# Optimization experiments

Measured on AMD Instinct MI355X. Metric: run time of the kernel, lower is better.

Reference implementation:

```python
import jax, jax.numpy as jnp
import numpy as np
import math

B, M, V, C, HID, BIN, H, W = 2, 1024, 300, 128, 128, 256, 384, 512


def fibonacci_sphere(n):
    # generate_grasp_views: n approximately-uniform directions on the unit sphere
    i = np.arange(n, dtype=np.float64)
    phi = (np.sqrt(5.0) - 1.0) / 2.0
    z = (2.0 * i + 1.0) / n - 1.0
    r = np.sqrt(np.maximum(1.0 - z * z, 0.0))
    t = 2.0 * np.pi * i * phi
    v = np.stack([r * np.cos(t), r * np.sin(t), z], -1)
    return (v / np.linalg.norm(v, axis=-1, keepdims=True)).astype(np.float32)


def setup_inputs():
    key = jax.random.key(0)
    ks = jax.random.split(key, 24)
    seed_features = jax.random.normal(ks[0], (B, C, M), jnp.float32)
    token_sel_idx = jax.random.randint(ks[1], (B, M), 0, H * W)
    fx = 525.0
    Kmat = jnp.array([[fx, 0.0, W / 2.0], [0.0, fx, H / 2.0], [0.0, 0.0, 1.0]], jnp.float32)
    K = jnp.broadcast_to(Kmat, (B, 3, 3))
    depth_map = 0.2 + 0.8 * jax.random.uniform(ks[2], (B, 1, H, W), jnp.float32)
    depth_prob = jax.nn.softmax(jax.random.normal(ks[3], (B, BIN, H, W), jnp.float32), axis=1)
    view_dirs = jnp.asarray(fibonacci_sphere(V))

    def lin(k, fan_in, shape):
        s = 1.0 / np.sqrt(fan_in)
        return jax.random.uniform(k, shape, jnp.float32, -s, s)

    qin = C + 7  # seed_feat + ray(3) + normal(3) + uncert(1)
    params = dict(
        Wq1=lin(ks[4], qin, (qin, HID)), bq1=lin(ks[5], qin, (HID,)),
        Wq2=lin(ks[6], HID, (HID, HID)), bq2=lin(ks[7], HID, (HID,)),
        Wa1=lin(ks[8], 3, (3, HID)), ba1=lin(ks[9], 3, (HID,)),
        Wa2=lin(ks[10], HID, (HID, HID)), ba2=lin(ks[11], HID, (HID,)),
        Wb1=lin(ks[12], 3, (3, HID // 2)), bb1=lin(ks[13], 3, (HID // 2,)),
        Wb2=lin(ks[14], HID // 2, (HID // 2, 1)), bb2=lin(ks[15], HID // 2, (1,)),
        Wr1=lin(ks[16], HID, (HID, C)), br1=lin(ks[17], HID, (C,)),
        Wr2=lin(ks[18], C, (C, C)), br2=lin(ks[19], C, (C,)),
    )
    return dict(seed_features=seed_features, token_sel_idx=token_sel_idx, K=K,
                depth_map=depth_map, depth_prob=depth_prob, view_dirs=view_dirs, **params)


def _views_to_rot(views):
    # batch_viewpoint_params_to_matrix(-views, angle=0)
    axis_x = -views
    zero = jnp.zeros_like(axis_x[..., 0])
    axis_y = jnp.stack([-axis_x[..., 1], axis_x[..., 0], zero], -1)
    ny = jnp.linalg.norm(axis_y, axis=-1, keepdims=True)
    fallback = jnp.broadcast_to(jnp.array([0.0, 1.0, 0.0], views.dtype), axis_y.shape)
    axis_y = jnp.where(ny < 1e-8, fallback, axis_y / jnp.maximum(ny, 1e-8))
    axis_x = axis_x / jnp.maximum(jnp.linalg.norm(axis_x, axis=-1, keepdims=True), 1e-8)
    axis_z = jnp.cross(axis_x, axis_y)
    return jnp.stack([axis_x, axis_y, axis_z], -1)  # (B,M,3,3)


def _forward(seed_features, token_sel_idx, K, depth_map, depth_prob, view_dirs,
             Wq1, bq1, Wq2, bq2, Wa1, ba1, Wa2, ba2, Wb1, bb1, Wb2, bb2, Wr1, br1, Wr2, br2):
    depth_map = jax.lax.stop_gradient(depth_map)   # .detach() in torch
    depth_prob = jax.lax.stop_gradient(depth_prob)
    # --- backproject depth to xyz map (B,3,H,W) ---
    ys, xs = jnp.meshgrid(jnp.arange(H, dtype=jnp.float32), jnp.arange(W, dtype=jnp.float32), indexing='ij')
    fx = K[:, 0, 0][:, None, None, None]; fy = K[:, 1, 1][:, None, None, None]
    cx = K[:, 0, 2][:, None, None, None]; cy = K[:, 1, 2][:, None, None, None]
    z = depth_map
    x = (xs[None, None] - cx) / fx * z
    y = (ys[None, None] - cy) / fy * z
    xyz = jnp.concatenate([x, y, z], axis=1)
    # --- central-difference normal map with replicate pad ---
    dx = (xyz[:, :, :, 2:] - xyz[:, :, :, :-2])[:, :, 1:-1, :]
    dy = (xyz[:, :, 2:, :] - xyz[:, :, :-2, :])[:, :, :, 1:-1]
    n = jnp.cross(dx.transpose(0, 2, 3, 1), dy.transpose(0, 2, 3, 1))
    n = n / jnp.maximum(jnp.linalg.norm(n, axis=-1, keepdims=True), 1e-6)
    normal_map = jnp.pad(n.transpose(0, 3, 1, 2), ((0, 0), (0, 0), (1, 1), (1, 1)), mode='edge')
    # --- depth uncertainty: normalized entropy over bins ---
    p = jnp.maximum(depth_prob, 1e-8)
    uncert_map = jnp.clip(-(p * jnp.log(p)).sum(axis=1, keepdims=True) / math.log(BIN), 0.0, 1.0)
    # --- per-seed irregular gathers ---
    def gather(feat, idx):
        Bf, Cf = feat.shape[0], feat.shape[1]
        flat = feat.reshape(Bf, Cf, H * W)
        return jnp.take_along_axis(flat, jnp.broadcast_to(idx[:, None, :], (Bf, Cf, idx.shape[1])), axis=2)
    normal_bm3 = gather(normal_map, token_sel_idx).transpose(0, 2, 1)  # (B,M,3)
    uncert_bm1 = gather(uncert_map, token_sel_idx).transpose(0, 2, 1)  # (B,M,1)
    u = (token_sel_idx % W).astype(jnp.float32)
    v = (token_sel_idx // W).astype(jnp.float32)
    rx = (u - K[:, 0, 2][:, None]) / K[:, 0, 0][:, None]
    ry = (v - K[:, 1, 2][:, None]) / K[:, 1, 1][:, None]
    rays = jnp.stack([rx, ry, jnp.ones_like(rx)], -1)
    rays = rays / jnp.maximum(jnp.linalg.norm(rays, axis=-1, keepdims=True), 1e-12)
    normal_bm3 = normal_bm3 * (1.0 - uncert_bm1)
    # --- query / anchor / bias MLPs ---
    q_in = jnp.concatenate([seed_features.transpose(0, 2, 1), rays, normal_bm3, uncert_bm1], -1)
    q = jax.nn.relu(jax.nn.relu(q_in @ Wq1 + bq1) @ Wq2 + bq2)          # (B,M,HID)
    a = jax.nn.relu(view_dirs @ Wa1 + ba1) @ Wa2 + ba2                  # (V,HID)
    bias = (jax.nn.relu(view_dirs @ Wb1 + bb1) @ Wb2 + bb2)[:, 0]        # (V,)
    logits = jnp.einsum('bmh,vh->bmv', q, a) / jnp.sqrt(jnp.float32(HID)) + bias
    view_score = jax.nn.sigmoid(logits)                                  # (B,M,V)
    # --- top-1 view selection + gather xyz / rot / anchor feat ---
    top_inds = jnp.argmax(view_score, axis=-1)                           # (B,M)
    top_xyz = view_dirs[top_inds]                                        # (B,M,3)
    rot = _views_to_rot(top_xyz)                                         # (B,M,3,3)
    top_a = a[top_inds]                                                  # (B,M,HID)
    res = jax.nn.relu((q + top_a) @ Wr1 + br1) @ Wr2 + br2               # (B,M,C)
    res_feat = res.transpose(0, 2, 1)                                    # (B,C,M)
    return view_score, top_inds, top_xyz, rot, res_feat


def reference(seed_features, token_sel_idx, K, depth_map, depth_prob, view_dirs,
              Wq1, bq1, Wq2, bq2, Wa1, ba1, Wa2, ba2, Wb1, bb1, Wb2, bb2, Wr1, br1, Wr2, br2):
    return _forward(seed_features, token_sel_idx, K, depth_map, depth_prob, view_dirs,
                    Wq1, bq1, Wq2, bq2, Wa1, ba1, Wa2, ba2, Wb1, bb1, Wb2, bb2, Wr1, br1, Wr2, br2)
```

## Files before the change

### kernel.cpp

```cpp
#include <hip/hip_runtime.h>
#include <math.h>

#define B 2
#define M 1024
#define V 300
#define C 128
#define HID 128
#define BIN 256
#define H 384
#define W 512
#define QIN (C + 7)
#define TM 8

__global__ __launch_bounds__(HID) void anchor_kernel(
    const float* __restrict__ view_dirs,
    const float* __restrict__ Wa1, const float* __restrict__ ba1,
    const float* __restrict__ Wa2, const float* __restrict__ ba2,
    const float* __restrict__ Wb1, const float* __restrict__ bb1,
    const float* __restrict__ Wb2, const float* __restrict__ bb2,
    float* __restrict__ a_out, float* __restrict__ aT_out,
    float* __restrict__ bias_out) {
  const int v = blockIdx.x;
  const int t = threadIdx.x;
  __shared__ float h1[HID];

  const float vd0 = view_dirs[v * 3 + 0];
  const float vd1 = view_dirs[v * 3 + 1];
  const float vd2 = view_dirs[v * 3 + 2];

  float h = vd0 * Wa1[0 * HID + t] + vd1 * Wa1[1 * HID + t] + vd2 * Wa1[2 * HID + t] + ba1[t];
  h1[t] = fmaxf(h, 0.0f);

  if (t < 64) {
    float x = vd0 * Wb1[0 * 64 + t] + vd1 * Wb1[1 * 64 + t] + vd2 * Wb1[2 * 64 + t] + bb1[t];
    x = fmaxf(x, 0.0f) * Wb2[t];
#pragma unroll
    for (int o = 32; o > 0; o >>= 1) x += __shfl_down(x, o, 64);
    if (t == 0) bias_out[v] = x + bb2[0];
  }
  __syncthreads();

  float acc = ba2[t];
#pragma unroll 8
  for (int k = 0; k < HID; ++k) acc += h1[k] * Wa2[k * HID + t];
  a_out[v * HID + t] = acc;
  aT_out[(size_t)t * V + v] = acc;
}

__global__ __launch_bounds__(256) void seed_kernel(
    const float* __restrict__ seed_features, const int* __restrict__ token_sel_idx,
    const float* __restrict__ Kmat, const float* __restrict__ depth_map,
    const float* __restrict__ depth_prob, const float* __restrict__ view_dirs,
    const float* __restrict__ Wq1, const float* __restrict__ bq1,
    const float* __restrict__ Wq2, const float* __restrict__ bq2,
    const float* __restrict__ Wr1, const float* __restrict__ br1,
    const float* __restrict__ Wr2, const float* __restrict__ br2,
    const float* __restrict__ a_ws, const float* __restrict__ aT_ws,
    const float* __restrict__ bias_ws,
    float* __restrict__ out_view_score, float* __restrict__ out_top_inds,
    float* __restrict__ out_top_xyz, float* __restrict__ out_rot,
    float* __restrict__ out_res) {
  const int bm0 = blockIdx.x * TM;
  const int b = bm0 / M;
  const int m0 = bm0 - b * M;
  const int t = threadIdx.x;
  const int lane = t & 63;
  const int wv = t >> 6;

  __shared__ float qin[TM][QIN + 1];
  __shared__ float hs[TM][HID];
  __shared__ float qs[TM][HID];
  __shared__ float sc_s[TM][304];
  __shared__ float atop[TM][HID];
  __shared__ float ered[TM];
  __shared__ int   sidx[TM];
  __shared__ int   sbest[TM];

  if (t < TM) sidx[t] = token_sel_idx[bm0 + t];

  for (int i = t; i < TM * C; i += 256) {
    const int s = i & 7;
    const int c = i >> 3;
    qin[s][c] = seed_features[((size_t)b * C + c) * M + m0 + s];
  }
  __syncthreads();

  {
    const int es = t >> 5;
    const int sub = t & 31;
    const float* dp = depth_prob + (size_t)b * BIN * H * W + sidx[es];
    float e = 0.0f;
#pragma unroll
    for (int j = 0; j < 8; ++j) {
      const float p = fmaxf(dp[(size_t)(sub + 32 * j) * (H * W)], 1e-8f);
      e += p * logf(p);
    }
#pragma unroll
    for (int o = 16; o > 0; o >>= 1) e += __shfl_down(e, o, 32);
    if (sub == 0) ered[es] = e;
  }
  __syncthreads();

  if (t < TM) {
    const int idx = sidx[t];
    float uncert = (-ered[t]) / 5.5451774444795623f;
    uncert = fminf(fmaxf(uncert, 0.0f), 1.0f);

    const float fx = Kmat[b * 9 + 0], fy = Kmat[b * 9 + 4];
    const float cx = Kmat[b * 9 + 2], cy = Kmat[b * 9 + 5];
    const int w = idx % W;
    const int h = idx / W;
    const int hc = min(max(h, 1), H - 2);
    const int wc = min(max(w, 1), W - 2);

    const float* dm = depth_map + (size_t)b * H * W;
    const float zl = dm[hc * W + (wc - 1)];
    const float zr = dm[hc * W + (wc + 1)];
    const float zu = dm[(hc - 1) * W + wc];
    const float zd = dm[(hc + 1) * W + wc];

    const float dxx = (wc + 1 - cx) / fx * zr - (wc - 1 - cx) / fx * zl;
    const float dxy = (hc - cy) / fy * zr - (hc - cy) / fy * zl;
    const float dxz = zr - zl;
    const float dyx = (wc - cx) / fx * zd - (wc - cx) / fx * zu;
    const float dyy = (hc + 1 - cy) / fy * zd - (hc - 1 - cy) / fy * zu;
    const float dyz = zd - zu;

    float nx = dxy * dyz - dxz * dyy;
    float ny = dxz * dyx - dxx * dyz;
    float nz = dxx * dyy - dxy * dyx;
    const float nn = fmaxf(sqrtf(nx * nx + ny * ny + nz * nz), 1e-6f);
    const float sc = (1.0f - uncert) / nn;

    const float rx = ((float)w - cx) / fx;
    const float ry = ((float)h - cy) / fy;
    const float rn = fmaxf(sqrtf(rx * rx + ry * ry + 1.0f), 1e-12f);

    qin[t][128] = rx / rn;
    qin[t][129] = ry / rn;
    qin[t][130] = 1.0f / rn;
    qin[t][131] = nx * sc;
    qin[t][132] = ny * sc;
    qin[t][133] = nz * sc;
    qin[t][134] = uncert;
  }
  __syncthreads();

  const int col = t & 127;
  const int grp = (t >> 7) * 4;
  {
    float acc0 = bq1[col], acc1 = acc0, acc2 = acc0, acc3 = acc0;
#pragma unroll 5
    for (int i = 0; i < QIN; ++i) {
      const float w = Wq1[i * HID + col];
      acc0 += qin[grp + 0][i] * w;
      acc1 += qin[grp + 1][i] * w;
      acc2 += qin[grp + 2][i] * w;
      acc3 += qin[grp + 3][i] * w;
    }
    hs[grp + 0][col] = fmaxf(acc0, 0.0f);
    hs[grp + 1][col] = fmaxf(acc1, 0.0f);
    hs[grp + 2][col] = fmaxf(acc2, 0.0f);
    hs[grp + 3][col] = fmaxf(acc3, 0.0f);
  }
  __syncthreads();

  {
    float acc0 = bq2[col], acc1 = acc0, acc2 = acc0, acc3 = acc0;
#pragma unroll 8
    for (int k = 0; k < HID; ++k) {
      const float w = Wq2[k * HID + col];
      acc0 += hs[grp + 0][k] * w;
      acc1 += hs[grp + 1][k] * w;
      acc2 += hs[grp + 2][k] * w;
      acc3 += hs[grp + 3][k] * w;
    }
    qs[grp + 0][col] = fmaxf(acc0, 0.0f);
    qs[grp + 1][col] = fmaxf(acc1, 0.0f);
    qs[grp + 2][col] = fmaxf(acc2, 0.0f);
    qs[grp + 3][col] = fmaxf(acc3, 0.0f);
  }
  __syncthreads();

  const float rsq = 0.08838834764831845f;
  for (int v = t; v < V; v += 256) {
    float d[TM];
#pragma unroll
    for (int s = 0; s < TM; ++s) d[s] = 0.0f;
#pragma unroll 4
    for (int k = 0; k < HID; ++k) {
      const float av = aT_ws[(size_t)k * V + v];
#pragma unroll
      for (int s = 0; s < TM; ++s) d[s] += qs[s][k] * av;
    }
    const float bsv = bias_ws[v];
#pragma unroll
    for (int s = 0; s < TM; ++s) {
      const float scv = 1.0f / (1.0f + expf(-(d[s] * rsq + bsv)));
      sc_s[s][v] = scv;
      out_view_score[(size_t)(bm0 + s) * V + v] = scv;
    }
  }
  __syncthreads();

  for (int s = wv; s < TM; s += 4) {
    float bv = -1.0f;
    int bi = 0;
    for (int v = lane; v < V; v += 64) {
      const float x = sc_s[s][v];
      if (x > bv) { bv = x; bi = v; }
    }
#pragma unroll
    for (int o = 32; o > 0; o >>= 1) {
      const float ov = __shfl_down(bv, o, 64);
      const int oi = __shfl_down(bi, o, 64);
      if (ov > bv || (ov == bv && oi < bi)) { bv = ov; bi = oi; }
    }
    if (lane == 0) sbest[s] = bi;
  }
  __syncthreads();

  if (t < TM) {
    const int best = sbest[t];
    const int bm = bm0 + t;
    out_top_inds[bm] = (float)best;
    const float vx = view_dirs[best * 3 + 0];
    const float vy = view_dirs[best * 3 + 1];
    const float vz = view_dirs[best * 3 + 2];
    out_top_xyz[(size_t)bm * 3 + 0] = vx;
    out_top_xyz[(size_t)bm * 3 + 1] = vy;
    out_top_xyz[(size_t)bm * 3 + 2] = vz;

    float ax0 = -vx, ax1 = -vy, ax2 = -vz;
    float ay0 = vy, ay1 = -vx, ay2 = 0.0f;
    const float nyn = sqrtf(ay0 * ay0 + ay1 * ay1);
    if (nyn < 1e-8f) {
      ay0 = 0.0f; ay1 = 1.0f; ay2 = 0.0f;
    } else {
      const float d = fmaxf(nyn, 1e-8f);
      ay0 /= d; ay1 /= d;
    }
    const float an = fmaxf(sqrtf(ax0 * ax0 + ax1 * ax1 + ax2 * ax2), 1e-8f);
    ax0 /= an; ax1 /= an; ax2 /= an;
    const float az0 = ax1 * ay2 - ax2 * ay1;
    const float az1 = ax2 * ay0 - ax0 * ay2;
    const float az2 = ax0 * ay1 - ax1 * ay0;
    float* R = out_rot + (size_t)bm * 9;
    R[0] = ax0; R[1] = ay0; R[2] = az0;
    R[3] = ax1; R[4] = ay1; R[5] = az1;
    R[6] = ax2; R[7] = ay2; R[8] = az2;
  }

  for (int i = t; i < TM * HID; i += 256) {
    const int s = i >> 7;
    const int k = i & 127;
    atop[s][k] = a_ws[(size_t)sbest[s] * HID + k];
  }
  __syncthreads();

  {
    float acc0 = br1[col], acc1 = acc0, acc2 = acc0, acc3 = acc0;
#pragma unroll 8
    for (int k = 0; k < HID; ++k) {
      const float w = Wr1[k * HID + col];
      acc0 += (qs[grp + 0][k] + atop[grp + 0][k]) * w;
      acc1 += (qs[grp + 1][k] + atop[grp + 1][k]) * w;
      acc2 += (qs[grp + 2][k] + atop[grp + 2][k]) * w;
      acc3 += (qs[grp + 3][k] + atop[grp + 3][k]) * w;
    }
    hs[grp + 0][col] = fmaxf(acc0, 0.0f);
    hs[grp + 1][col] = fmaxf(acc1, 0.0f);
    hs[grp + 2][col] = fmaxf(acc2, 0.0f);
    hs[grp + 3][col] = fmaxf(acc3, 0.0f);
  }
  __syncthreads();

  {
    float acc0 = br2[col], acc1 = acc0, acc2 = acc0, acc3 = acc0;
#pragma unroll 8
    for (int k = 0; k < HID; ++k) {
      const float w = Wr2[k * HID + col];
      acc0 += hs[grp + 0][k] * w;
      acc1 += hs[grp + 1][k] * w;
      acc2 += hs[grp + 2][k] * w;
      acc3 += hs[grp + 3][k] * w;
    }
    float* o = out_res + ((size_t)b * C + col) * M + m0 + grp;
    o[0] = acc0; o[1] = acc1; o[2] = acc2; o[3] = acc3;
  }
}

extern "C" void kernel_launch(void* const* d_in, const int* in_sizes, int n_in,
                              void* d_out, int out_size, void* d_ws, size_t ws_size,
                              hipStream_t stream) {
  const float* seed  = (const float*)d_in[0];
  const int*   tok   = (const int*)d_in[1];
  const float* Km    = (const float*)d_in[2];
  const float* dmap  = (const float*)d_in[3];
  const float* dprob = (const float*)d_in[4];
  const float* vdirs = (const float*)d_in[5];
  const float* Wq1 = (const float*)d_in[6];  const float* bq1 = (const float*)d_in[7];
  const float* Wq2 = (const float*)d_in[8];  const float* bq2 = (const float*)d_in[9];
  const float* Wa1 = (const float*)d_in[10]; const float* ba1 = (const float*)d_in[11];
  const float* Wa2 = (const float*)d_in[12]; const float* ba2 = (const float*)d_in[13];
  const float* Wb1 = (const float*)d_in[14]; const float* bb1 = (const float*)d_in[15];
  const float* Wb2 = (const float*)d_in[16]; const float* bb2 = (const float*)d_in[17];
  const float* Wr1 = (const float*)d_in[18]; const float* br1 = (const float*)d_in[19];
  const float* Wr2 = (const float*)d_in[20]; const float* br2 = (const float*)d_in[21];

  float* out = (float*)d_out;
  float* vs  = out;
  float* ti  = vs + (size_t)B * M * V;
  float* tx  = ti + (size_t)B * M;
  float* rot = tx + (size_t)B * M * 3;
  float* rf  = rot + (size_t)B * M * 9;

  float* a_ws    = (float*)d_ws;
  float* aT_ws   = a_ws + (size_t)V * HID;
  float* bias_ws = aT_ws + (size_t)HID * V;

  anchor_kernel<<<V, HID, 0, stream>>>(vdirs, Wa1, ba1, Wa2, ba2, Wb1, bb1, Wb2, bb2,
                                       a_ws, aT_ws, bias_ws);
  seed_kernel<<<(B * M) / TM, 256, 0, stream>>>(seed, tok, Km, dmap, dprob, vdirs,
                                                Wq1, bq1, Wq2, bq2, Wr1, br1, Wr2, br2,
                                                a_ws, aT_ws, bias_ws, vs, ti, tx, rot, rf);
}
```

Baseline: 558.4 us.

## Split depth-entropy and geometry computation into a separate per-seed kernel

Moves the depth-probability entropy, surface normal and ray computation out of the MLP kernel into a new geo_kernel with one 256-thread block per seed. Each thread does one strided gather of depth_prob, which gives far more blocks and memory parallelism for these scattered loads than the 8-seeds-per-block layout did. The MLP kernel now reads the 7 extra features from a workspace buffer. This adds a kernel launch and a small round trip through global memory.

```diff
diff --git a/kernel.cpp b/kernel.cpp
--- a/kernel.cpp
+++ b/kernel.cpp
@@ -11,6 +11,76 @@
 #define W 512
 #define QIN (C + 7)
 #define TM 8
+
+__global__ __launch_bounds__(256) void geo_kernel(
+    const int* __restrict__ token_sel_idx, const float* __restrict__ Kmat,
+    const float* __restrict__ depth_map, const float* __restrict__ depth_prob,
+    float* __restrict__ extras) {
+  const int bm = blockIdx.x;
+  const int b = bm >> 10;
+  const int t = threadIdx.x;
+  const int lane = t & 63;
+  const int wv = t >> 6;
+
+  __shared__ float ered[4];
+  __shared__ int sidx_s;
+  if (t == 0) sidx_s = token_sel_idx[bm];
+  __syncthreads();
+  const int idx = sidx_s;
+
+  {
+    const float p = fmaxf(depth_prob[(size_t)b * BIN * H * W + (size_t)t * (H * W) + idx], 1e-8f);
+    float e = p * logf(p);
+#pragma unroll
+    for (int o = 32; o > 0; o >>= 1) e += __shfl_down(e, o, 64);
+    if (lane == 0) ered[wv] = e;
+  }
+  __syncthreads();
+
+  if (t == 0) {
+    float uncert = (-(ered[0] + ered[1] + ered[2] + ered[3])) / 5.5451774444795623f;
+    uncert = fminf(fmaxf(uncert, 0.0f), 1.0f);
+
+    const float fx = Kmat[b * 9 + 0], fy = Kmat[b * 9 + 4];
+    const float cx = Kmat[b * 9 + 2], cy = Kmat[b * 9 + 5];
+    const int w = idx % W;
+    const int h = idx / W;
+    const int hc = min(max(h, 1), H - 2);
+    const int wc = min(max(w, 1), W - 2);
+
+    const float* dm = depth_map + (size_t)b * H * W;
+    const float zl = dm[hc * W + (wc - 1)];
+    const float zr = dm[hc * W + (wc + 1)];
+    const float zu = dm[(hc - 1) * W + wc];
+    const float zd = dm[(hc + 1) * W + wc];
+
+    const float dxx = (wc + 1 - cx) / fx * zr - (wc - 1 - cx) / fx * zl;
+    const float dxy = (hc - cy) / fy * zr - (hc - cy) / fy * zl;
+    const float dxz = zr - zl;
+    const float dyx = (wc - cx) / fx * zd - (wc - cx) / fx * zu;
+    const float dyy = (hc + 1 - cy) / fy * zd - (hc - 1 - cy) / fy * zu;
+    const float dyz = zd - zu;
+
+    float nx = dxy * dyz - dxz * dyy;
+    float ny = dxz * dyx - dxx * dyz;
+    float nz = dxx * dyy - dxy * dyx;
+    const float nn = fmaxf(sqrtf(nx * nx + ny * ny + nz * nz), 1e-6f);
+    const float sc = (1.0f - uncert) / nn;
+
+    const float rx = ((float)w - cx) / fx;
+    const float ry = ((float)h - cy) / fy;
+    const float rn = fmaxf(sqrtf(rx * rx + ry * ry + 1.0f), 1e-12f);
+
+    float* e8 = extras + (size_t)bm * 8;
+    e8[0] = rx / rn;
+    e8[1] = ry / rn;
+    e8[2] = 1.0f / rn;
+    e8[3] = nx * sc;
+    e8[4] = ny * sc;
+    e8[5] = nz * sc;
+    e8[6] = uncert;
+  }
+}
 
 __global__ __launch_bounds__(HID) void anchor_kernel(
     const float* __restrict__ view_dirs,
@@ -47,10 +117,9 @@
   aT_out[(size_t)t * V + v] = acc;
 }
 
-__global__ __launch_bounds__(256) void seed_kernel(
-    const float* __restrict__ seed_features, const int* __restrict__ token_sel_idx,
-    const float* __restrict__ Kmat, const float* __restrict__ depth_map,
-    const float* __restrict__ depth_prob, const float* __restrict__ view_dirs,
+__global__ __launch_bounds__(256) void seed_mlp_kernel(
+    const float* __restrict__ seed_features, const float* __restrict__ extras,
+    const float* __restrict__ view_dirs,
     const float* __restrict__ Wq1, const float* __restrict__ bq1,
     const float* __restrict__ Wq2, const float* __restrict__ bq2,
     const float* __restrict__ Wr1, const float* __restrict__ br1,
@@ -61,7 +130,7 @@
     float* __restrict__ out_top_xyz, float* __restrict__ out_rot,
     float* __restrict__ out_res) {
   const int bm0 = blockIdx.x * TM;
-  const int b = bm0 / M;
+  const int b = bm0 >> 10;
   const int m0 = bm0 - b * M;
   const int t = threadIdx.x;
   const int lane = t & 63;
@@ -72,82 +141,23 @@
   __shared__ float qs[TM][HID];
   __shared__ float sc_s[TM][304];
   __shared__ float atop[TM][HID];
-  __shared__ float ered[TM];
-  __shared__ int   sidx[TM];
   __shared__ int   sbest[TM];
-
-  if (t < TM) sidx[t] = token_sel_idx[bm0 + t];
 
   for (int i = t; i < TM * C; i += 256) {
     const int s = i & 7;
     const int c = i >> 3;
     qin[s][c] = seed_features[((size_t)b * C + c) * M + m0 + s];
   }
-  __syncthreads();
-
-  {
-    const int es = t >> 5;
-    const int sub = t & 31;
-    const float* dp = depth_prob + (size_t)b * BIN * H * W + sidx[es];
-    float e = 0.0f;
-#pragma unroll
-    for (int j = 0; j < 8; ++j) {
-      const float p = fmaxf(dp[(size_t)(sub + 32 * j) * (H * W)], 1e-8f);
-      e += p * logf(p);
-    }
-#pragma unroll
-    for (int o = 16; o > 0; o >>= 1) e += __shfl_down(e, o, 32);
-    if (sub == 0) ered[es] = e;
-  }
-  __syncthreads();
-
-  if (t < TM) {
-    const int idx = sidx[t];
-    float uncert = (-ered[t]) / 5.5451774444795623f;
-    uncert = fminf(fmaxf(uncert, 0.0f), 1.0f);
-
-    const float fx = Kmat[b * 9 + 0], fy = Kmat[b * 9 + 4];
-    const float cx = Kmat[b * 9 + 2], cy = Kmat[b * 9 + 5];
-    const int w = idx % W;
-    const int h = idx / W;
-    const int hc = min(max(h, 1), H - 2);
-    const int wc = min(max(w, 1), W - 2);
-
-    const float* dm = depth_map + (size_t)b * H * W;
-    const float zl = dm[hc * W + (wc - 1)];
-    const float zr = dm[hc * W + (wc + 1)];
-    const float zu = dm[(hc - 1) * W + wc];
-    const float zd = dm[(hc + 1) * W + wc];
-
-    const float dxx = (wc + 1 - cx) / fx * zr - (wc - 1 - cx) / fx * zl;
-    const float dxy = (hc - cy) / fy * zr - (hc - cy) / fy * zl;
-    const float dxz = zr - zl;
-    const float dyx = (wc - cx) / fx * zd - (wc - cx) / fx * zu;
-    const float dyy = (hc + 1 - cy) / fy * zd - (hc - 1 - cy) / fy * zu;
-    const float dyz = zd - zu;
-
-    float nx = dxy * dyz - dxz * dyy;
-    float ny = dxz * dyx - dxx * dyz;
-    float nz = dxx * dyy - dxy * dyx;
-    const float nn = fmaxf(sqrtf(nx * nx + ny * ny + nz * nz), 1e-6f);
-    const float sc = (1.0f - uncert) / nn;
-
-    const float rx = ((float)w - cx) / fx;
-    const float ry = ((float)h - cy) / fy;
-    const float rn = fmaxf(sqrtf(rx * rx + ry * ry + 1.0f), 1e-12f);
-
-    qin[t][128] = rx / rn;
-    qin[t][129] = ry / rn;
-    qin[t][130] = 1.0f / rn;
-    qin[t][131] = nx * sc;
-    qin[t][132] = ny * sc;
-    qin[t][133] = nz * sc;
-    qin[t][134] = uncert;
+  if (t < TM * 8) {
+    const int s = t >> 3;
+    const int j = t & 7;
+    if (j < 7) qin[s][128 + j] = extras[(size_t)(bm0 + s) * 8 + j];
   }
   __syncthreads();
 
   const int col = t & 127;
   const int grp = (t >> 7) * 4;
+
   {
     float acc0 = bq1[col], acc1 = acc0, acc2 = acc0, acc3 = acc0;
 #pragma unroll 5
@@ -318,10 +328,12 @@
   float* a_ws    = (float*)d_ws;
   float* aT_ws   = a_ws + (size_t)V * HID;
   float* bias_ws = aT_ws + (size_t)HID * V;
-
+  float* extras  = bias_ws + V + 4;
+
+  geo_kernel<<<B * M, 256, 0, stream>>>(tok, Km, dmap, dprob, extras);
   anchor_kernel<<<V, HID, 0, stream>>>(vdirs, Wa1, ba1, Wa2, ba2, Wb1, bb1, Wb2, bb2,
                                        a_ws, aT_ws, bias_ws);
-  seed_kernel<<<(B * M) / TM, 256, 0, stream>>>(seed, tok, Km, dmap, dprob, vdirs,
-                                                Wq1, bq1, Wq2, bq2, Wr1, br1, Wr2, br2,
-                                                a_ws, aT_ws, bias_ws, vs, ti, tx, rot, rf);
+  seed_mlp_kernel<<<(B * M) / TM, 256, 0, stream>>>(seed, extras, vdirs,
+                                                    Wq1, bq1, Wq2, bq2, Wr1, br1, Wr2, br2,
+                                                    a_ws, aT_ws, bias_ws, vs, ti, tx, rot, rf);
 }
```

New measurement: 563.3 us. About the same (+0.9%).
